# Optimization experiments

Measured on AMD Instinct MI355X. Metric: run time of the kernel, lower is better.

## Reference

```python
import jax, jax.numpy as jnp
import numpy as np

COORD_W, EDGE_W, COUNT_W, REG_W, CONTRA_W = 1.0, 2.0, 0.1, 0.001, 0.1
MARGIN = 1.0


def setup_inputs() -> dict:
    key = jax.random.key(0)
    ks = jax.random.split(key, 6)
    B, N, D, C = 16, 1024, 128, 2
    return {
        "predicted_coords": jax.random.normal(ks[0], (B, N, C), jnp.float32),
        "points": jax.random.normal(ks[1], (B, N, C), jnp.float32),
        "adjacency_logits": jax.random.normal(ks[2], (B, N, N), jnp.float32),
        "adjacency": jax.random.bernoulli(ks[3], 0.1, (B, N, N)).astype(jnp.float32),
        "node_masks": jnp.ones((B, N), jnp.float32),  # all nodes valid -> n_actual = N
        "predicted_count": jax.random.normal(ks[4], (B, 1), jnp.float32),
        "node_features": jax.random.normal(ks[5], (B, N, D), jnp.float32),
    }


def _bce_with_logits(logits, targets):
    # mean-reduced, numerically stable (matches F.binary_cross_entropy_with_logits)
    return jnp.mean(jnp.maximum(logits, 0.0) - logits * targets
                    + jnp.log1p(jnp.exp(-jnp.abs(logits))))


def _smooth_l1(pred, target):
    d = jnp.abs(pred - target)
    return jnp.mean(jnp.where(d < 1.0, 0.5 * d * d, d - 0.5))


def _contrastive_sample(features, adj):
    # features: [N, D], adj: [N, N]. torch.cdist pairwise euclidean via gram trick.
    nrm = jnp.sum(features * features, axis=-1)              # [N]
    sq = jnp.maximum(nrm[:, None] + nrm[None, :]
                     - 2.0 * (features @ features.T), 0.0)   # [N, N] squared dists
    n = features.shape[0]
    eye = jnp.eye(n, dtype=bool)
    pos_mask = adj > 0.5
    neg_mask = (adj <= 0.5) & (~eye)
    # positive term: mean of distances**2 over positive pairs == mean squared dist
    pos = jnp.sum(jnp.where(pos_mask, sq, 0.0)) / jnp.maximum(jnp.sum(pos_mask), 1)
    dist = jnp.sqrt(jnp.maximum(sq, 1e-12))
    hinge = jnp.square(jax.nn.relu(MARGIN - dist))
    neg = jnp.sum(jnp.where(neg_mask, hinge, 0.0)) / jnp.maximum(jnp.sum(neg_mask), 1)
    return pos + neg


def reference(predicted_coords, points, adjacency_logits, adjacency,
              node_masks, predicted_count, node_features):
    # node_masks are all ones, so the per-sample [:n_actual] slicing is the
    # full tensor; per-sample MSE/BCE means averaged over batch equal global means.
    coord_loss = jnp.mean(jnp.square(predicted_coords - points))
    edge_loss = _bce_with_logits(adjacency_logits, adjacency)
    actual_counts = jnp.sum(node_masks, axis=1)              # [B]
    count_loss = _smooth_l1(predicted_count[:, 0], actual_counts)
    reg_loss = jnp.mean(jnp.square(node_features))
    # contrastive path uses targets['adjacency'] (no predicted_adjacency key)
    contra_loss = jnp.mean(jax.vmap(_contrastive_sample)(node_features, adjacency))
    total = (COORD_W * coord_loss + EDGE_W * edge_loss + COUNT_W * count_loss
             + REG_W * reg_loss + CONTRA_W * contra_loss)
    return total, coord_loss, edge_loss, count_loss, reg_loss, contra_loss
```

## Files before the change

kernel.cpp:

```cpp
#include <hip/hip_runtime.h>
#include <hip/hip_bf16.h>

#define NN    1024
#define DD    128
#define TILE  128
#define PITCH 136
#define SQP   132
#define NBLK  1024

typedef __bf16 bf16_t;
typedef bf16_t bf16x8 __attribute__((ext_vector_type(8)));
typedef float  f32x4  __attribute__((ext_vector_type(4)));
typedef _Float16 half4 __attribute__((ext_vector_type(4)));


__global__ __launch_bounds__(256) void small_losses(
    const float* __restrict__ pcoord, const float* __restrict__ pts,
    const float* __restrict__ masks,  const float* __restrict__ pcount,
    float* __restrict__ ws) {
  __shared__ float sh[4][2];
  float coord = 0.f, cnt = 0.f;
  const int gt = blockIdx.x * 256 + threadIdx.x;
  const int stride = 16 * 256;

  const float4* a4 = (const float4*)pcoord;
  const float4* b4 = (const float4*)pts;
  for (int i = gt; i < 8192; i += stride) {
    float4 a = a4[i], b = b4[i];
    float dx = a.x-b.x, dy = a.y-b.y, dz = a.z-b.z, dw = a.w-b.w;
    coord += dx*dx + dy*dy + dz*dz + dw*dw;
  }
  const float* m = masks + blockIdx.x * NN;
  for (int i = threadIdx.x; i < NN; i += 256) cnt += m[i];

  const int lane = threadIdx.x & 63, w = threadIdx.x >> 6;
  #pragma unroll
  for (int o = 32; o; o >>= 1) {
    coord += __shfl_xor(coord, o);
    cnt   += __shfl_xor(cnt, o);
  }
  if (lane == 0) { sh[w][0] = coord; sh[w][1] = cnt; }
  __syncthreads();
  if (threadIdx.x == 0) {
    float c = 0.f, n = 0.f;
    for (int i = 0; i < 4; ++i) { c += sh[i][0]; n += sh[i][1]; }
    atomicAdd(&ws[0], c);
    float d = fabsf(pcount[blockIdx.x] - n);
    float term = (d < 1.f) ? 0.5f * d * d : d - 0.5f;
    atomicAdd(&ws[2], term);
  }
}

__device__ __forceinline__ void loss_elem(float l, float a, float s, bool offd,
    float& bsum, float& poss, float& posc, float& negs) {
  bsum += fmaxf(l, 0.f) - l * a + __logf(1.f + __expf(-fabsf(l)));
  const bool pos = a > 0.5f;
  poss += pos ? s : 0.f;
  posc += pos ? 1.f : 0.f;
  if (!pos && offd && s < 1.f) {
    float d = sqrtf(fmaxf(s, 1e-12f));
    float h = 1.f - d;
    negs += h * h;
  }
}

__global__ __launch_bounds__(512, 4) void gram_sq(
    const float* __restrict__ feat, _Float16* __restrict__ sqout,
    float* __restrict__ ws) {
  __shared__ __align__(16) char smem[2 * TILE * PITCH * sizeof(bf16_t)];
  bf16_t* lsA = (bf16_t*)smem;
  bf16_t* lsB = (bf16_t*)(smem + TILE * PITCH * sizeof(bf16_t));
  float*  sqb = (float*)smem;
  __shared__ float nrmA[TILE], nrmB[TILE];
  __shared__ float red[8];

  const int bx  = blockIdx.x;
  const int b   = bx >> 6;
  const int tid = bx & 63;
  const int ti  = (tid >> 3) << 7;
  const int tj  = (tid & 7)  << 7;
  const bool diag = ((tid >> 3) == (tid & 7));

  const int t = threadIdx.x;
  const float* fb = feat + (size_t)b * NN * DD;

  float regsum = 0.f;
  #pragma unroll
  for (int it = 0; it < 8; ++it) {
    int cid  = it * 512 + t;
    int tile = cid >> 11;
    int sub  = cid & 2047;
    int row  = sub >> 4;
    int c8   = sub & 15;
    const float* src = fb + (size_t)((tile ? tj : ti) + row) * DD + c8 * 8;
    float4 u = *(const float4*)src;
    float4 v = *(const float4*)(src + 4);
    if (diag && tile == 0)
      regsum += u.x*u.x + u.y*u.y + u.z*u.z + u.w*u.w
              + v.x*v.x + v.y*v.y + v.z*v.z + v.w*v.w;
    bf16_t* dst = (tile ? lsB : lsA) + row * PITCH + c8 * 8;
    dst[0] = (bf16_t)u.x; dst[1] = (bf16_t)u.y; dst[2] = (bf16_t)u.z; dst[3] = (bf16_t)u.w;
    dst[4] = (bf16_t)v.x; dst[5] = (bf16_t)v.y; dst[6] = (bf16_t)v.z; dst[7] = (bf16_t)v.w;
  }
  __syncthreads();

  {
    int row  = t >> 1;
    int half = t & 1;
    const bf16_t* src = (row < TILE ? lsA + row * PITCH : lsB + (row - TILE) * PITCH)
                        + half * 64;
    float s = 0.f;
    #pragma unroll
    for (int c = 0; c < 8; ++c) {
      bf16x8 ch = *(const bf16x8*)(src + c * 8);
      #pragma unroll
      for (int i = 0; i < 8; ++i) { float v = (float)ch[i]; s += v * v; }
    }
    s += __shfl_xor(s, 1);
    if (half == 0) { if (row < TILE) nrmA[row] = s; else nrmB[row - TILE] = s; }
  }

  const int lane = t & 63;
  const int wave = t >> 6;
  const int lrow = lane & 15;
  const int quad = lane >> 4;

  f32x4 acc[8];
  #pragma unroll
  for (int fc = 0; fc < 8; ++fc) acc[fc] = (f32x4){0.f, 0.f, 0.f, 0.f};

  #pragma unroll
  for (int k0 = 0; k0 < DD; k0 += 32) {
    const int kc = k0 + quad * 8;
    bf16x8 aF = *(const bf16x8*)&lsA[(wave * 16 + lrow) * PITCH + kc];
    bf16x8 bF[8];
    #pragma unroll
    for (int fc = 0; fc < 8; ++fc)
      bF[fc] = *(const bf16x8*)&lsB[(fc * 16 + lrow) * PITCH + kc];
    #pragma unroll
    for (int fc = 0; fc < 8; ++fc)
      acc[fc] = __builtin_amdgcn_mfma_f32_16x16x32_bf16(aF, bF[fc], acc[fc], 0, 0, 0);
  }
  __syncthreads();

  {
    const int rbase = wave * 16 + quad * 4;
    #pragma unroll
    for (int fc = 0; fc < 8; ++fc) {
      const int ctile = fc * 16 + lrow;
      const float ncol = nrmB[ctile];
      #pragma unroll
      for (int r = 0; r < 4; ++r) {
        const int rtile = rbase + r;
        sqb[rtile * SQP + ctile] = fmaxf(nrmA[rtile] + ncol - 2.f * acc[fc][r], 0.f);
      }
    }
  }
  __syncthreads();

  {
    const int c4 = t & 31, r0 = t >> 5;
    _Float16* sb = sqout + (size_t)b * NN * NN + (size_t)(ti + r0) * NN + tj + c4 * 4;
    for (int it = 0; it < 8; ++it) {
      float4 s = *(const float4*)&sqb[(it * 16 + r0) * SQP + c4 * 4];
      half4 h = { (_Float16)s.x, (_Float16)s.y, (_Float16)s.z, (_Float16)s.w };
      *(half4*)(sb + (size_t)it * 16 * NN) = h;
    }
  }

  if (diag) {
    #pragma unroll
    for (int o = 32; o; o >>= 1) regsum += __shfl_xor(regsum, o);
    if (lane == 0) red[wave] = regsum;
    __syncthreads();
    if (t == 0) {
      float s = 0.f;
      for (int w = 0; w < 8; ++w) s += red[w];
      atomicAdd(&ws[1], s);
    }
  }
}

__global__ __launch_bounds__(256) void bce_stream(
    const float* __restrict__ logits, const float* __restrict__ adj,
    const _Float16* __restrict__ sq, float* __restrict__ ws) {
  __shared__ float red[4][4];
  const int b   = blockIdx.x >> 7;
  const int blk = blockIdx.x & 127;
  const int t   = threadIdx.x;
  const int row0 = blk * 8;
  const size_t base = (size_t)b * NN * NN + (size_t)row0 * NN;
  const float4* lp = (const float4*)(logits + base);
  const float4* ap = (const float4*)(adj + base);
  const half4*  sp = (const half4*)(sq + base);

  float bsum = 0.f, poss = 0.f, posc = 0.f, negs = 0.f;
  #pragma unroll 2
  for (int i = t; i < 2048; i += 256) {
    float4 L = lp[i];
    float4 A = ap[i];
    half4  S = sp[i];
    const int grow  = row0 + (i >> 8);
    const int gcol0 = (i & 255) * 4;
    loss_elem(L.x, A.x, (float)S[0], grow != gcol0 + 0, bsum, poss, posc, negs);
    loss_elem(L.y, A.y, (float)S[1], grow != gcol0 + 1, bsum, poss, posc, negs);
    loss_elem(L.z, A.z, (float)S[2], grow != gcol0 + 2, bsum, poss, posc, negs);
    loss_elem(L.w, A.w, (float)S[3], grow != gcol0 + 3, bsum, poss, posc, negs);
  }

  const int lane = t & 63, wave = t >> 6;
  #pragma unroll
  for (int o = 32; o; o >>= 1) {
    bsum += __shfl_xor(bsum, o);
    poss += __shfl_xor(poss, o);
    posc += __shfl_xor(posc, o);
    negs += __shfl_xor(negs, o);
  }
  if (lane == 0) {
    red[wave][0] = bsum; red[wave][1] = poss;
    red[wave][2] = posc; red[wave][3] = negs;
  }
  __syncthreads();
  if (t == 0) {
    float s0=0.f,s1=0.f,s2=0.f,s3=0.f;
    for (int w = 0; w < 4; ++w) {
      s0 += red[w][0]; s1 += red[w][1]; s2 += red[w][2]; s3 += red[w][3];
    }
    atomicAdd(&ws[3], s0);
    atomicAdd(&ws[4 + b], s1);
    atomicAdd(&ws[20 + b], s2);
    atomicAdd(&ws[36 + b], s3);
  }
}

__global__ void finalize(const float* __restrict__ ws, float* __restrict__ out) {
  if (threadIdx.x != 0 || blockIdx.x != 0) return;
  float coord = ws[0] / 32768.f;
  float reg   = ws[1] / 2097152.f;
  float cntl  = ws[2] / 16.f;
  float edge  = ws[3] / 16777216.f;
  float contra = 0.f;
  for (int b = 0; b < 16; ++b) {
    float negcnt = 1048576.f - 1024.f - ws[20 + b];
    float p = ws[4 + b]  / fmaxf(ws[20 + b], 1.f);
    float n = ws[36 + b] / fmaxf(negcnt, 1.f);
    contra += p + n;
  }
  contra *= (1.f / 16.f);
  float total = coord + 2.f * edge + 0.1f * cntl + 0.001f * reg + 0.1f * contra;
  out[0] = total; out[1] = coord; out[2] = edge;
  out[3] = cntl;  out[4] = reg;   out[5] = contra;
}

extern "C" void kernel_launch(void* const* d_in, const int* in_sizes, int n_in,
                              void* d_out, int out_size, void* d_ws, size_t ws_size,
                              hipStream_t stream) {
  (void)in_sizes; (void)n_in; (void)out_size;
  const float* pcoord = (const float*)d_in[0];
  const float* pts    = (const float*)d_in[1];
  const float* logits = (const float*)d_in[2];
  const float* adj    = (const float*)d_in[3];
  const float* masks  = (const float*)d_in[4];
  const float* pcount = (const float*)d_in[5];
  const float* nf     = (const float*)d_in[6];
  float* ws  = (float*)d_ws;
  float* out = (float*)d_out;

  hipMemsetAsync(ws, 0, 68 * sizeof(float), stream);
  small_losses<<<16, 256, 0, stream>>>(pcoord, pts, masks, pcount, ws);
  _Float16* sqbuf = (_Float16*)((char*)d_ws + 1024);
  gram_sq<<<NBLK, 512, 0, stream>>>(nf, sqbuf, ws);
  bce_stream<<<2048, 256, 0, stream>>>(logits, adj, sqbuf, ws);
  finalize<<<1, 64, 0, stream>>>(ws, out);
}
```

Measured before the change: 226.6 us.

## Double-buffer BCE stream via async LDS loads and make the inner loop branch-free

The streaming loss kernel now stages logits, adjacency and squared-distance tiles into shared memory with global_load_lds, double-buffered across 8 chunks, so the next chunk loads while the current one is computed. The per-element diagonal test and the divergent negative-hinge branch are removed. The diagonal is instead zeroed in the gram output, and its contribution is corrected in finalize using diagonal positive counts gathered in small_losses. This adds two barriers per chunk and extra shared memory, and moves some correction logic elsewhere.

```diff
diff --git a/kernel.cpp b/kernel.cpp
--- a/kernel.cpp
+++ b/kernel.cpp
@@ -14,53 +14,53 @@
 typedef _Float16 half4 __attribute__((ext_vector_type(4)));
 
 
+__device__ __forceinline__ void async_load16(const void* g, void* l) {
+  __builtin_amdgcn_global_load_lds(
+      (const __attribute__((address_space(1))) void*)g,
+      (__attribute__((address_space(3))) void*)l, 16, 0, 0);
+}
+
 __global__ __launch_bounds__(256) void small_losses(
     const float* __restrict__ pcoord, const float* __restrict__ pts,
     const float* __restrict__ masks,  const float* __restrict__ pcount,
-    float* __restrict__ ws) {
-  __shared__ float sh[4][2];
-  float coord = 0.f, cnt = 0.f;
-  const int gt = blockIdx.x * 256 + threadIdx.x;
+    const float* __restrict__ adj,    float* __restrict__ ws) {
+  __shared__ float sh[4][3];
+  float coord = 0.f, cnt = 0.f, pd = 0.f;
+  const int b = blockIdx.x;
+  const int gt = b * 256 + threadIdx.x;
   const int stride = 16 * 256;
 
   const float4* a4 = (const float4*)pcoord;
   const float4* b4 = (const float4*)pts;
   for (int i = gt; i < 8192; i += stride) {
-    float4 a = a4[i], b = b4[i];
-    float dx = a.x-b.x, dy = a.y-b.y, dz = a.z-b.z, dw = a.w-b.w;
+    float4 a = a4[i], bb = b4[i];
+    float dx = a.x-bb.x, dy = a.y-bb.y, dz = a.z-bb.z, dw = a.w-bb.w;
     coord += dx*dx + dy*dy + dz*dz + dw*dw;
   }
-  const float* m = masks + blockIdx.x * NN;
-  for (int i = threadIdx.x; i < NN; i += 256) cnt += m[i];
+  const float* m = masks + b * NN;
+  const float* ad = adj + (size_t)b * NN * NN;
+  for (int i = threadIdx.x; i < NN; i += 256) {
+    cnt += m[i];
+    pd  += (ad[(size_t)i * (NN + 1)] > 0.5f) ? 1.f : 0.f;
+  }
 
   const int lane = threadIdx.x & 63, w = threadIdx.x >> 6;
   #pragma unroll
   for (int o = 32; o; o >>= 1) {
     coord += __shfl_xor(coord, o);
     cnt   += __shfl_xor(cnt, o);
-  }
-  if (lane == 0) { sh[w][0] = coord; sh[w][1] = cnt; }
+    pd    += __shfl_xor(pd, o);
+  }
+  if (lane == 0) { sh[w][0] = coord; sh[w][1] = cnt; sh[w][2] = pd; }
   __syncthreads();
   if (threadIdx.x == 0) {
-    float c = 0.f, n = 0.f;
-    for (int i = 0; i < 4; ++i) { c += sh[i][0]; n += sh[i][1]; }
+    float c = 0.f, n = 0.f, p = 0.f;
+    for (int i = 0; i < 4; ++i) { c += sh[i][0]; n += sh[i][1]; p += sh[i][2]; }
     atomicAdd(&ws[0], c);
-    float d = fabsf(pcount[blockIdx.x] - n);
+    float d = fabsf(pcount[b] - n);
     float term = (d < 1.f) ? 0.5f * d * d : d - 0.5f;
     atomicAdd(&ws[2], term);
-  }
-}
-
-__device__ __forceinline__ void loss_elem(float l, float a, float s, bool offd,
-    float& bsum, float& poss, float& posc, float& negs) {
-  bsum += fmaxf(l, 0.f) - l * a + __logf(1.f + __expf(-fabsf(l)));
-  const bool pos = a > 0.5f;
-  poss += pos ? s : 0.f;
-  posc += pos ? 1.f : 0.f;
-  if (!pos && offd && s < 1.f) {
-    float d = sqrtf(fmaxf(s, 1e-12f));
-    float h = 1.f - d;
-    negs += h * h;
+    ws[68 + b] = p;
   }
 }
 
@@ -163,6 +163,10 @@
     _Float16* sb = sqout + (size_t)b * NN * NN + (size_t)(ti + r0) * NN + tj + c4 * 4;
     for (int it = 0; it < 8; ++it) {
       float4 s = *(const float4*)&sqb[(it * 16 + r0) * SQP + c4 * 4];
+      if (diag) {
+        int cc = (it * 16 + r0) - c4 * 4;
+        if (cc >= 0 && cc < 4) ((float*)&s)[cc] = 0.f;
+      }
       half4 h = { (_Float16)s.x, (_Float16)s.y, (_Float16)s.z, (_Float16)s.w };
       *(half4*)(sb + (size_t)it * 16 * NN) = h;
     }
@@ -184,29 +188,50 @@
 __global__ __launch_bounds__(256) void bce_stream(
     const float* __restrict__ logits, const float* __restrict__ adj,
     const _Float16* __restrict__ sq, float* __restrict__ ws) {
+  __shared__ __align__(16) char smem[2][10240];
   __shared__ float red[4][4];
+
   const int b   = blockIdx.x >> 7;
   const int blk = blockIdx.x & 127;
   const int t   = threadIdx.x;
-  const int row0 = blk * 8;
-  const size_t base = (size_t)b * NN * NN + (size_t)row0 * NN;
-  const float4* lp = (const float4*)(logits + base);
-  const float4* ap = (const float4*)(adj + base);
-  const half4*  sp = (const half4*)(sq + base);
+  const int wv  = t >> 6;
+  const size_t base = (size_t)b * NN * NN + (size_t)(blk * 8) * NN;
+  const char* lpB = (const char*)(logits + base);
+  const char* apB = (const char*)(adj + base);
+  const char* spB = (const char*)(sq + base);
+
+  #define STAGE(c, p)                                                   \
+    do {                                                                \
+      async_load16(lpB + (c) * 4096 + t * 16, smem[p] + wv * 1024);     \
+      async_load16(apB + (c) * 4096 + t * 16, smem[p] + 4096 + wv * 1024); \
+      if (t < 128)                                                      \
+        async_load16(spB + (c) * 2048 + t * 16, smem[p] + 8192 + wv * 1024); \
+    } while (0)
 
   float bsum = 0.f, poss = 0.f, posc = 0.f, negs = 0.f;
-  #pragma unroll 2
-  for (int i = t; i < 2048; i += 256) {
-    float4 L = lp[i];
-    float4 A = ap[i];
-    half4  S = sp[i];
-    const int grow  = row0 + (i >> 8);
-    const int gcol0 = (i & 255) * 4;
-    loss_elem(L.x, A.x, (float)S[0], grow != gcol0 + 0, bsum, poss, posc, negs);
-    loss_elem(L.y, A.y, (float)S[1], grow != gcol0 + 1, bsum, poss, posc, negs);
-    loss_elem(L.z, A.z, (float)S[2], grow != gcol0 + 2, bsum, poss, posc, negs);
-    loss_elem(L.w, A.w, (float)S[3], grow != gcol0 + 3, bsum, poss, posc, negs);
-  }
+  STAGE(0, 0);
+  for (int c = 0; c < 8; ++c) {
+    const int p = c & 1;
+    if (c < 7) STAGE(c + 1, p ^ 1);
+    __syncthreads();
+    float4 L = *(const float4*)(smem[p] + t * 16);
+    float4 A = *(const float4*)(smem[p] + 4096 + t * 16);
+    half4  S = *(const half4*)(smem[p] + 8192 + t * 8);
+    #pragma unroll
+    for (int k = 0; k < 4; ++k) {
+      float l = ((const float*)&L)[k];
+      float a = ((const float*)&A)[k];
+      float s = (float)S[k];
+      bsum += fmaxf(l, 0.f) - l * a + __logf(1.f + __expf(-fabsf(l)));
+      float h = fmaxf(1.f - sqrtf(fmaxf(s, 1e-12f)), 0.f);
+      bool pos = a > 0.5f;
+      poss += pos ? s : 0.f;
+      posc += pos ? 1.f : 0.f;
+      negs += pos ? 0.f : h * h;
+    }
+    __syncthreads();
+  }
+  #undef STAGE
 
   const int lane = t & 63, wave = t >> 6;
   #pragma unroll
@@ -239,11 +264,16 @@
   float reg   = ws[1] / 2097152.f;
   float cntl  = ws[2] / 16.f;
   float edge  = ws[3] / 16777216.f;
+  float kk = fmaxf(1.f - sqrtf(fmaxf(0.f, 1e-12f)), 0.f);
+  kk = kk * kk;
   float contra = 0.f;
   for (int b = 0; b < 16; ++b) {
-    float negcnt = 1048576.f - 1024.f - ws[20 + b];
-    float p = ws[4 + b]  / fmaxf(ws[20 + b], 1.f);
-    float n = ws[36 + b] / fmaxf(negcnt, 1.f);
+    float posdiag = ws[68 + b];
+    float posc    = ws[20 + b];
+    float negcnt  = 1048576.f - 1024.f - posc + posdiag;
+    float negsum  = ws[36 + b] - (1024.f - posdiag) * kk;
+    float p = ws[4 + b] / fmaxf(posc, 1.f);
+    float n = negsum / fmaxf(negcnt, 1.f);
     contra += p + n;
   }
   contra *= (1.f / 16.f);
@@ -255,7 +285,7 @@
 extern "C" void kernel_launch(void* const* d_in, const int* in_sizes, int n_in,
                               void* d_out, int out_size, void* d_ws, size_t ws_size,
                               hipStream_t stream) {
-  (void)in_sizes; (void)n_in; (void)out_size;
+  (void)in_sizes; (void)n_in; (void)out_size; (void)ws_size;
   const float* pcoord = (const float*)d_in[0];
   const float* pts    = (const float*)d_in[1];
   const float* logits = (const float*)d_in[2];
@@ -266,8 +296,8 @@
   float* ws  = (float*)d_ws;
   float* out = (float*)d_out;
 
-  hipMemsetAsync(ws, 0, 68 * sizeof(float), stream);
-  small_losses<<<16, 256, 0, stream>>>(pcoord, pts, masks, pcount, ws);
+  hipMemsetAsync(ws, 0, 84 * sizeof(float), stream);
+  small_losses<<<16, 256, 0, stream>>>(pcoord, pts, masks, pcount, adj, ws);
   _Float16* sqbuf = (_Float16*)((char*)d_ws + 1024);
   gram_sq<<<NBLK, 512, 0, stream>>>(nf, sqbuf, ws);
   bce_stream<<<2048, 256, 0, stream>>>(logits, adj, sqbuf, ws);
```

After: 254.4 us. 1.12x slower.
